# Performance work log

Hardware: AMD Instinct MI355X
Metric: run time of the kernel (lower is better)

The kernel has to match this reference:

```python
import jax, jax.numpy as jnp
import numpy as np


def _fir_kernel():
    # StyleGAN-2 low-pass FIR: outer([1,3,3,1]) normalized to sum 1
    k1 = jnp.array([1.0, 3.0, 3.0, 1.0], dtype=jnp.float32)
    k2 = jnp.outer(k1, k1)
    return k2 / k2.sum()


def setup_inputs() -> dict:
    key = jax.random.key(0)
    kx, kw = jax.random.split(key, 2)
    B, H, W, C, OC = 8, 128, 128, 128, 128
    x = jax.random.normal(kx, (B, H, W, C), dtype=jnp.float32)
    conv_w = jax.random.normal(kw, (3, 3, C, OC), dtype=jnp.float32) * 0.02  # HWIO
    conv_b = jnp.zeros((OC,), dtype=jnp.float32)
    return {"x": x, "conv_w": conv_w, "conv_b": conv_b}


def _upsample_fir(x):
    B, H, W, C = x.shape
    kernel = _fir_kernel()
    x_up = jnp.zeros((B, 2 * H, 2 * W, C), dtype=x.dtype)
    x_up = x_up.at[:, ::2, ::2, :].set(x)
    k = jnp.tile(kernel[None, None, :, :], (C, 1, 1, 1))  # OIHW, O=C, I=1
    y = jax.lax.conv_general_dilated(
        jnp.transpose(x_up, (0, 3, 1, 2)),  # NCHW
        k * 4.0,
        window_strides=(1, 1),
        padding="SAME",
        feature_group_count=C,
    )
    return jnp.transpose(y, (0, 2, 3, 1))  # back to NHWC


def reference(x, conv_w, conv_b):
    x_up = _upsample_fir(x)  # (B, 2H, 2W, C)
    out = jax.lax.conv_general_dilated(
        x_up,
        conv_w,
        window_strides=(1, 1),
        padding="SAME",
        dimension_numbers=("NHWC", "HWIO", "NHWC"),
    )
    return out + conv_b
```

## Files before the change

### kernel.cpp

```cpp
#include <hip/hip_runtime.h>

typedef __bf16 bf16x8 __attribute__((ext_vector_type(8)));
typedef float f32x4 __attribute__((ext_vector_type(4)));
typedef unsigned short ushort8 __attribute__((ext_vector_type(8)));

__device__ __forceinline__ unsigned short f2bf(float f) {
  unsigned int u = __builtin_bit_cast(unsigned int, f);
  u += 0x7FFFu + ((u >> 16) & 1u);
  return (unsigned short)(u >> 16);
}

__constant__ float COEF[2][3][3] = {
    {{0.25f, 0.00f, 0.00f},
     {0.75f, 0.75f, 0.25f},
     {0.00f, 0.25f, 0.75f}},
    {{0.75f, 0.25f, 0.00f},
     {0.25f, 0.75f, 0.75f},
     {0.00f, 0.00f, 0.25f}}
};

__global__ void pack_weights(const float* __restrict__ w, unsigned short* __restrict__ pw) {
  const int kt = blockIdx.x >> 3, nt = blockIdx.x & 7;
  const int l = threadIdx.x;
  const int tap = kt >> 2, cblk = kt & 3;
  const int du = tap / 3, dv = tap - du * 3;
  const int c0 = cblk * 32 + ((l >> 4) << 3);
  const int oc = nt * 16 + (l & 15);
  float accp[4][8];
#pragma unroll
  for (int ph = 0; ph < 4; ++ph)
#pragma unroll
    for (int j = 0; j < 8; ++j) accp[ph][j] = 0.0f;
#pragma unroll
  for (int u = 0; u < 3; ++u)
#pragma unroll
    for (int v = 0; v < 3; ++v) {
      const float ra0 = COEF[0][du][u], ra1 = COEF[1][du][u];
      const float cb0 = COEF[0][dv][v], cb1 = COEF[1][dv][v];
      const float c00 = ra0 * cb0, c01 = ra0 * cb1, c10 = ra1 * cb0, c11 = ra1 * cb1;
#pragma unroll
      for (int j = 0; j < 8; ++j) {
        const float wv = w[((u * 3 + v) * 128 + c0 + j) * 128 + oc];
        accp[0][j] += c00 * wv;
        accp[1][j] += c01 * wv;
        accp[2][j] += c10 * wv;
        accp[3][j] += c11 * wv;
      }
    }
  const int fi = ((cblk * 3 + dv) * 3 + du) * 8 + nt;
#pragma unroll
  for (int ph = 0; ph < 4; ++ph) {
    ushort8 o;
#pragma unroll
    for (int j = 0; j < 8; ++j) o[j] = f2bf(accp[ph][j]);
    *(ushort8*)(pw + (((ph * 288 + fi) * 64 + l) << 3)) = o;
  }
}

__global__ __launch_bounds__(512, 2) void fused_all(
    const float* __restrict__ x, const unsigned short* __restrict__ pw,
    const float* __restrict__ w, const float* __restrict__ bias,
    float* __restrict__ out) {
  __shared__ __align__(16) char smem[11 * 19 * 256];

  const int bid = blockIdx.x;
  const int tid = threadIdx.x;

  if (bid < 512) {
    const int chunk = bid & 31;
    const int type = (bid >> 5) & 1;
    const int bi = bid >> 6;
    const int base0 = chunk * 8;
    const float* xb = x + bi * (128 * 128 * 128);

    float* yw = (float*)smem;
    float* part = (float*)(smem + 16384);

    {
      const int c = tid & 127;
      const int sub = tid >> 7;
      for (int k = sub; k < 20; k += 4) {
        const int f = k / 10;
        const int ws = k - f * 10;
        const int t = base0 - 1 + ws;
        float val = 0.0f;
        if ((unsigned)t < 256u) {
          const int t0 = t >> 1;
          const float hA0 = (t & 1) ? 0.25f : 0.75f;
          const float hA1 = 1.0f - hA0;
          const float hF0 = f ? 0.25f : 0.75f;
          const float hF1 = 1.0f - hF0;
          const bool ok = (t0 + 1) < 128;
          if (type == 0) {
            const float v00 = xb[t0 * 128 + c];
            const float v01 = ok ? xb[(t0 + 1) * 128 + c] : 0.0f;
            const float v10 = xb[(128 + t0) * 128 + c];
            const float v11 = ok ? xb[(128 + t0 + 1) * 128 + c] : 0.0f;
            val = hF0 * (hA0 * v00 + hA1 * v01) + hF1 * (hA0 * v10 + hA1 * v11);
          } else {
            const float v00 = xb[(t0 * 128) * 128 + c];
            const float v01 = xb[(t0 * 128 + 1) * 128 + c];
            const float v10 = ok ? xb[((t0 + 1) * 128) * 128 + c] : 0.0f;
            const float v11 = ok ? xb[((t0 + 1) * 128 + 1) * 128 + c] : 0.0f;
            val = hA0 * (hF0 * v00 + hF1 * v01) + hA1 * (hF0 * v10 + hF1 * v11);
          }
        }
        yw[(f * 10 + ws) * 128 + c] = val;
      }
    }
    __syncthreads();

    const int wv = tid >> 6;
    const int oc0 = (tid & 63) * 2;
    const int cbase = wv * 16;

    float acc[8][2] = {};
#pragma unroll 1
    for (int cc = 0; cc < 16; ++cc) {
      float yr[2][10];
#pragma unroll
      for (int f = 0; f < 2; ++f)
#pragma unroll
        for (int ws = 0; ws < 10; ++ws)
          yr[f][ws] = yw[(f * 10 + ws) * 128 + cbase + cc];
#pragma unroll
      for (int tf = 0; tf < 2; ++tf) {
#pragma unroll
        for (int tb = 0; tb < 3; ++tb) {
          const int uu = (type == 0) ? (tf + 1) : tb;
          const int vv = (type == 0) ? tb : (tf + 1);
          const float2 w2 = *(const float2*)(
              w + ((uu * 3 + vv) * 128 + cbase + cc) * 128 + oc0);
#pragma unroll
          for (int pos = 0; pos < 8; ++pos) {
            const float yv = yr[tf][pos + tb];
            acc[pos][0] += yv * w2.x;
            acc[pos][1] += yv * w2.y;
          }
        }
      }
    }

#pragma unroll
    for (int pos = 0; pos < 8; ++pos)
      *(float2*)(part + (wv * 8 + pos) * 128 + oc0) = *(float2*)acc[pos];
    __syncthreads();

    const int pos = tid >> 6;
    const int ocp = (tid & 63) * 2;
    float s0 = 0.0f, s1 = 0.0f;
#pragma unroll
    for (int w8 = 0; w8 < 8; ++w8) {
      const float2 v = *(const float2*)(part + (w8 * 8 + pos) * 128 + ocp);
      s0 += v.x; s1 += v.y;
    }
    const int posg = base0 + pos;
    if (!(type == 1 && posg == 0)) {
      const int p = (type == 0) ? 0 : posg;
      const int q = (type == 0) ? posg : 0;
      const float2 b2 = *(const float2*)(bias + ocp);
      float2 r; r.x = s0 + b2.x; r.y = s1 + b2.y;
      *(float2*)(out + bi * (256 * 256 * 128) + (p * 256 + q) * 128 + ocp) = r;
    }
    return;
  }

  char* xlds = smem;
  const int o = bid - 512;
  const int blk = (o & 7) * 128 + (o >> 3);
  const int bimg = blk >> 7;
  const int it = (blk >> 3) & 15;
  const int jt = blk & 7;
  const int I0 = it * 8, J0 = jt * 16;
  const float* xb = x + bimg * (128 * 128 * 128);

  const int lane = tid & 63;
  const int l15 = lane & 15;
  const int lh = lane >> 4;
  const int wid = tid >> 6;
  const int a = (wid >> 2) & 1;
  const int b = (wid >> 1) & 1;
  const int nhalf = wid & 1;
  const int ph = a * 2 + b;

  const char* pwb = (const char*)pw + ph * 294912 + nhalf * 4096 + lane * 16;

#define LOADB(buf, g_, du_)                                           \
  do {                                                                \
    const char* bp_ = pwb + (((g_) * 3 + (du_)) << 13);               \
    _Pragma("unroll") for (int n = 0; n < 4; ++n)                     \
        buf[n] = *(const bf16x8*)(bp_ + n * 1024);                    \
  } while (0)

  bf16x8 b0[4], b1[4], b2[4];
  LOADB(b0, 0, 0);

  for (int idx = tid; idx < 11 * 19 * 16; idx += 512) {
    const int cp = idx & 15;
    const int pos = idx >> 4;
    const int xr = pos / 19;
    const int xc = pos - xr * 19;
    const int gi = I0 - 1 + xr;
    const int gj = J0 - 1 + xc;
    ushort8 u8 = {};
    if (((unsigned)gi < 128u) && ((unsigned)gj < 128u)) {
      const float* p = xb + ((gi << 7) + gj) * 128 + (cp << 3);
      const float4 A = *(const float4*)p;
      const float4 Bv = *(const float4*)(p + 4);
      u8[0] = f2bf(A.x); u8[1] = f2bf(A.y); u8[2] = f2bf(A.z); u8[3] = f2bf(A.w);
      u8[4] = f2bf(Bv.x); u8[5] = f2bf(Bv.y); u8[6] = f2bf(Bv.z); u8[7] = f2bf(Bv.w);
    }
    int byte = (pos << 8) + (cp << 4);
    byte ^= (pos & 7) << 4;
    *(ushort8*)(xlds + byte) = u8;
  }
  __syncthreads();

  f32x4 acc[8][4] = {};
  const int colpart = l15 + b;

#pragma unroll 1
  for (int g = 0; g < 12; ++g) {
    const int cblk = (g * 11) >> 5;
    const int dv = g - cblk * 3;
    const int kbyte = (cblk * 4 + lh) << 4;
    const int pbase = a * 19 + colpart + dv;

    bf16x8 af[10];
#define AREAD(rr)                                                     \
    do {                                                              \
      const int posa = pbase + (rr) * 19;                             \
      int byte_ = (posa << 8) + kbyte;                                \
      byte_ ^= (posa & 7) << 4;                \
      af[rr] = *(const bf16x8*)(xlds + byte_);                        \
    } while (0)

    AREAD(0); AREAD(1); AREAD(2); AREAD(3);
    AREAD(4); AREAD(5); AREAD(6); AREAD(7);
    LOADB(b1, g, 1);
    AREAD(8); AREAD(9);
    LOADB(b2, g, 2);

    __builtin_amdgcn_s_setprio(1);
#pragma unroll
    for (int m = 0; m < 8; ++m)
#pragma unroll
      for (int n = 0; n < 4; ++n)
        acc[m][n] = __builtin_amdgcn_mfma_f32_16x16x32_bf16(af[m], b0[n], acc[m][n], 0, 0, 0);
    __builtin_amdgcn_s_setprio(0);

    {
      const int gn = (g < 11) ? (g + 1) : 11;
      LOADB(b0, gn, 0);
    }

    __builtin_amdgcn_s_setprio(1);
#pragma unroll
    for (int m = 0; m < 8; ++m)
#pragma unroll
      for (int n = 0; n < 4; ++n)
        acc[m][n] = __builtin_amdgcn_mfma_f32_16x16x32_bf16(af[m + 1], b1[n], acc[m][n], 0, 0, 0);

#pragma unroll
    for (int m = 0; m < 8; ++m)
#pragma unroll
      for (int n = 0; n < 4; ++n)
        acc[m][n] = __builtin_amdgcn_mfma_f32_16x16x32_bf16(af[m + 2], b2[n], acc[m][n], 0, 0, 0);
    __builtin_amdgcn_s_setprio(0);
#undef AREAD
  }
#undef LOADB

  float bv[4];
#pragma unroll
  for (int n = 0; n < 4; ++n) bv[n] = bias[nhalf * 64 + n * 16 + l15];
  float* ob = out + bimg * (256 * 256 * 128) + nhalf * 64 + l15;
#pragma unroll
  for (int m = 0; m < 8; ++m) {
    const int p = it * 16 + 2 * m + a;
    if (p == 0) continue;
#pragma unroll
    for (int jr = 0; jr < 4; ++jr) {
      const int q = jt * 32 + 2 * (lh * 4 + jr) + b;
      if (q == 0) continue;
      float* orow = ob + (p * 256 + q) * 128;
#pragma unroll
      for (int n = 0; n < 4; ++n) orow[n * 16] = acc[m][n][jr] + bv[n];
    }
  }
}

extern "C" void kernel_launch(void* const* d_in, const int* in_sizes, int n_in,
                              void* d_out, int out_size, void* d_ws, size_t ws_size,
                              hipStream_t stream) {
  const float* x = (const float*)d_in[0];
  const float* w = (const float*)d_in[1];
  const float* bias = (const float*)d_in[2];
  float* out = (float*)d_out;
  unsigned short* pw = (unsigned short*)d_ws;

  pack_weights<<<dim3(288), dim3(64), 0, stream>>>(w, pw);
  fused_all<<<dim3(1536), dim3(512), 0, stream>>>(x, pw, w, bias, out);
}
```

Before: 172.1 us.

## Halve row tile to 256-thread blocks, each wave covering all 128 output channels

Shrinks the main conv tile from 8 to 4 input rows with 256-thread blocks (4 waves) instead of 512. Each wave now computes all 128 output channels (8 N-fragments) over 4 M-rows rather than splitting channels across wave pairs. The weight prefetch becomes a two-buffer ping-pong across an unrolled pair of groups. The aim is less LDS per block, more blocks for load balance, and more B reuse per A read. In exchange, each wave holds more accumulator and weight registers, and each block carries a larger relative halo in the x tile.

```diff
diff --git a/kernel.cpp b/kernel.cpp
--- a/kernel.cpp
+++ b/kernel.cpp
@@ -57,11 +57,11 @@
   }
 }
 
-__global__ __launch_bounds__(512, 2) void fused_all(
+__global__ __launch_bounds__(256, 2) void fused_all(
     const float* __restrict__ x, const unsigned short* __restrict__ pw,
     const float* __restrict__ w, const float* __restrict__ bias,
     float* __restrict__ out) {
-  __shared__ __align__(16) char smem[11 * 19 * 256];
+  __shared__ __align__(16) char smem[7 * 19 * 256];
 
   const int bid = blockIdx.x;
   const int tid = threadIdx.x;
@@ -74,12 +74,12 @@
     const float* xb = x + bi * (128 * 128 * 128);
 
     float* yw = (float*)smem;
-    float* part = (float*)(smem + 16384);
+    float* part = (float*)(smem + 10240);
 
     {
       const int c = tid & 127;
       const int sub = tid >> 7;
-      for (int k = sub; k < 20; k += 4) {
+      for (int k = sub; k < 20; k += 2) {
         const int f = k / 10;
         const int ws = k - f * 10;
         const int t = base0 - 1 + ws;
@@ -112,11 +112,11 @@
 
     const int wv = tid >> 6;
     const int oc0 = (tid & 63) * 2;
-    const int cbase = wv * 16;
+    const int cbase = wv * 32;
 
     float acc[8][2] = {};
 #pragma unroll 1
-    for (int cc = 0; cc < 16; ++cc) {
+    for (int cc = 0; cc < 32; ++cc) {
       float yr[2][10];
 #pragma unroll
       for (int f = 0; f < 2; ++f)
@@ -146,56 +146,56 @@
       *(float2*)(part + (wv * 8 + pos) * 128 + oc0) = *(float2*)acc[pos];
     __syncthreads();
 
-    const int pos = tid >> 6;
-    const int ocp = (tid & 63) * 2;
-    float s0 = 0.0f, s1 = 0.0f;
-#pragma unroll
-    for (int w8 = 0; w8 < 8; ++w8) {
-      const float2 v = *(const float2*)(part + (w8 * 8 + pos) * 128 + ocp);
-      s0 += v.x; s1 += v.y;
+    const int pos = tid >> 5;
+    const int ocp = (tid & 31) * 4;
+    float4 s = {0.f, 0.f, 0.f, 0.f};
+#pragma unroll
+    for (int w4i = 0; w4i < 4; ++w4i) {
+      const float4 v = *(const float4*)(part + (w4i * 8 + pos) * 128 + ocp);
+      s.x += v.x; s.y += v.y; s.z += v.z; s.w += v.w;
     }
     const int posg = base0 + pos;
     if (!(type == 1 && posg == 0)) {
       const int p = (type == 0) ? 0 : posg;
       const int q = (type == 0) ? posg : 0;
-      const float2 b2 = *(const float2*)(bias + ocp);
-      float2 r; r.x = s0 + b2.x; r.y = s1 + b2.y;
-      *(float2*)(out + bi * (256 * 256 * 128) + (p * 256 + q) * 128 + ocp) = r;
+      const float4 b4 = *(const float4*)(bias + ocp);
+      float4 r;
+      r.x = s.x + b4.x; r.y = s.y + b4.y; r.z = s.z + b4.z; r.w = s.w + b4.w;
+      *(float4*)(out + bi * (256 * 256 * 128) + (p * 256 + q) * 128 + ocp) = r;
     }
     return;
   }
 
   char* xlds = smem;
   const int o = bid - 512;
-  const int blk = (o & 7) * 128 + (o >> 3);
-  const int bimg = blk >> 7;
-  const int it = (blk >> 3) & 15;
+  const int blk = (o & 7) * 256 + (o >> 3);
+  const int bimg = blk >> 8;
+  const int it = (blk >> 3) & 31;
   const int jt = blk & 7;
-  const int I0 = it * 8, J0 = jt * 16;
+  const int I0 = it * 4, J0 = jt * 16;
   const float* xb = x + bimg * (128 * 128 * 128);
 
   const int lane = tid & 63;
   const int l15 = lane & 15;
   const int lh = lane >> 4;
   const int wid = tid >> 6;
-  const int a = (wid >> 2) & 1;
-  const int b = (wid >> 1) & 1;
-  const int nhalf = wid & 1;
+  const int a = wid >> 1;
+  const int b = wid & 1;
   const int ph = a * 2 + b;
 
-  const char* pwb = (const char*)pw + ph * 294912 + nhalf * 4096 + lane * 16;
+  const char* pwb = (const char*)pw + ph * 294912 + lane * 16;
 
 #define LOADB(buf, g_, du_)                                           \
   do {                                                                \
     const char* bp_ = pwb + (((g_) * 3 + (du_)) << 13);               \
-    _Pragma("unroll") for (int n = 0; n < 4; ++n)                     \
+    _Pragma("unroll") for (int n = 0; n < 8; ++n)                     \
         buf[n] = *(const bf16x8*)(bp_ + n * 1024);                    \
   } while (0)
 
-  bf16x8 b0[4], b1[4], b2[4];
-  LOADB(b0, 0, 0);
-
-  for (int idx = tid; idx < 11 * 19 * 16; idx += 512) {
+  bf16x8 bX[8], bY[8];
+  LOADB(bX, 0, 0);
+
+  for (int idx = tid; idx < 7 * 19 * 16; idx += 256) {
     const int cp = idx & 15;
     const int pos = idx >> 4;
     const int xr = pos / 19;
@@ -216,68 +216,73 @@
   }
   __syncthreads();
 
-  f32x4 acc[8][4] = {};
+  f32x4 acc[4][8] = {};
   const int colpart = l15 + b;
 
+#define AREAD(rr, dv_)                                                \
+  do {                                                                \
+    const int posa = (a + (rr)) * 19 + colpart + (dv_);               \
+    int byte_ = (posa << 8) + kbyte;                                  \
+    byte_ ^= (posa & 7) << 4;                  \
+    af[rr] = *(const bf16x8*)(xlds + byte_);                          \
+  } while (0)
+
+#define MFMAS(du_, buf)                                               \
+  do {                                                                \
+    __builtin_amdgcn_s_setprio(1);                                    \
+    _Pragma("unroll") for (int m = 0; m < 4; ++m)                     \
+        _Pragma("unroll") for (int n = 0; n < 8; ++n)                 \
+            acc[m][n] = __builtin_amdgcn_mfma_f32_16x16x32_bf16(      \
+                af[(du_) + m], buf[n], acc[m][n], 0, 0, 0);           \
+    __builtin_amdgcn_s_setprio(0);                                    \
+  } while (0)
+
 #pragma unroll 1
-  for (int g = 0; g < 12; ++g) {
-    const int cblk = (g * 11) >> 5;
-    const int dv = g - cblk * 3;
-    const int kbyte = (cblk * 4 + lh) << 4;
-    const int pbase = a * 19 + colpart + dv;
-
-    bf16x8 af[10];
-#define AREAD(rr)                                                     \
-    do {                                                              \
-      const int posa = pbase + (rr) * 19;                             \
-      int byte_ = (posa << 8) + kbyte;                                \
-      byte_ ^= (posa & 7) << 4;                \
-      af[rr] = *(const bf16x8*)(xlds + byte_);                        \
-    } while (0)
-
-    AREAD(0); AREAD(1); AREAD(2); AREAD(3);
-    AREAD(4); AREAD(5); AREAD(6); AREAD(7);
-    LOADB(b1, g, 1);
-    AREAD(8); AREAD(9);
-    LOADB(b2, g, 2);
-
-    __builtin_amdgcn_s_setprio(1);
-#pragma unroll
-    for (int m = 0; m < 8; ++m)
-#pragma unroll
-      for (int n = 0; n < 4; ++n)
-        acc[m][n] = __builtin_amdgcn_mfma_f32_16x16x32_bf16(af[m], b0[n], acc[m][n], 0, 0, 0);
-    __builtin_amdgcn_s_setprio(0);
-
+  for (int g = 0; g < 12; g += 2) {
     {
-      const int gn = (g < 11) ? (g + 1) : 11;
-      LOADB(b0, gn, 0);
-    }
-
-    __builtin_amdgcn_s_setprio(1);
-#pragma unroll
-    for (int m = 0; m < 8; ++m)
-#pragma unroll
-      for (int n = 0; n < 4; ++n)
-        acc[m][n] = __builtin_amdgcn_mfma_f32_16x16x32_bf16(af[m + 1], b1[n], acc[m][n], 0, 0, 0);
-
-#pragma unroll
-    for (int m = 0; m < 8; ++m)
-#pragma unroll
-      for (int n = 0; n < 4; ++n)
-        acc[m][n] = __builtin_amdgcn_mfma_f32_16x16x32_bf16(af[m + 2], b2[n], acc[m][n], 0, 0, 0);
-    __builtin_amdgcn_s_setprio(0);
+      const int cblk = (g * 11) >> 5;
+      const int dv = g - cblk * 3;
+      const int kbyte = (cblk * 4 + lh) << 4;
+      bf16x8 af[6];
+      AREAD(0, dv); AREAD(1, dv); AREAD(2, dv);
+      AREAD(3, dv); AREAD(4, dv); AREAD(5, dv);
+      LOADB(bY, g, 1);
+      MFMAS(0, bX);
+      LOADB(bX, g, 2);
+      MFMAS(1, bY);
+      LOADB(bY, g + 1, 0);
+      MFMAS(2, bX);
+    }
+    {
+      const int g1 = g + 1;
+      const int cblk = (g1 * 11) >> 5;
+      const int dv = g1 - cblk * 3;
+      const int kbyte = (cblk * 4 + lh) << 4;
+      bf16x8 af[6];
+      AREAD(0, dv); AREAD(1, dv); AREAD(2, dv);
+      AREAD(3, dv); AREAD(4, dv); AREAD(5, dv);
+      LOADB(bX, g1, 1);
+      MFMAS(0, bY);
+      LOADB(bY, g1, 2);
+      MFMAS(1, bX);
+      {
+        const int gn = (g + 2 < 12) ? (g + 2) : 11;
+        LOADB(bX, gn, 0);
+      }
+      MFMAS(2, bY);
+    }
+  }
 #undef AREAD
-  }
+#undef MFMAS
 #undef LOADB
 
-  float bv[4];
-#pragma unroll
-  for (int n = 0; n < 4; ++n) bv[n] = bias[nhalf * 64 + n * 16 + l15];
-  float* ob = out + bimg * (256 * 256 * 128) + nhalf * 64 + l15;
-#pragma unroll
-  for (int m = 0; m < 8; ++m) {
-    const int p = it * 16 + 2 * m + a;
+  float bv[8];
+#pragma unroll
+  for (int n = 0; n < 8; ++n) bv[n] = bias[n * 16 + l15];
+  float* ob = out + bimg * (256 * 256 * 128) + l15;
+#pragma unroll
+  for (int m = 0; m < 4; ++m) {
+    const int p = it * 8 + 2 * m + a;
     if (p == 0) continue;
 #pragma unroll
     for (int jr = 0; jr < 4; ++jr) {
@@ -285,7 +290,7 @@
       if (q == 0) continue;
       float* orow = ob + (p * 256 + q) * 128;
 #pragma unroll
-      for (int n = 0; n < 4; ++n) orow[n * 16] = acc[m][n][jr] + bv[n];
+      for (int n = 0; n < 8; ++n) orow[n * 16] = acc[m][n][jr] + bv[n];
     }
   }
 }
@@ -300,5 +305,5 @@
   unsigned short* pw = (unsigned short*)d_ws;
 
   pack_weights<<<dim3(288), dim3(64), 0, stream>>>(w, pw);
-  fused_all<<<dim3(1536), dim3(512), 0, stream>>>(x, pw, w, bias, out);
+  fused_all<<<dim3(2560), dim3(256), 0, stream>>>(x, pw, w, bias, out);
 }
```

New measurement: 178.1 us. 3.5% more time.

## Switch main conv to 32x32x16 MFMA with 4x32 spatial tiles

Applied to the files above, without the earlier changes.

The main conv path moves from 16x16x32 bf16 MFMA to 32x32x16 MFMA. Each block now covers a 4x32 input tile (a 7x35 halo in LDS) instead of 8x16, and the K loop is split into 24 half-steps. The pre-packed weight layout is reorganised to match the new B-fragment shape. The goal is fewer LDS A-fragment reads per FLOP and higher MFMA efficiency, at the cost of a wider halo, a slightly larger LDS footprint, and changed output store patterns.

```diff
diff --git a/kernel.cpp b/kernel.cpp
--- a/kernel.cpp
+++ b/kernel.cpp
@@ -1,7 +1,7 @@
 #include <hip/hip_runtime.h>
 
 typedef __bf16 bf16x8 __attribute__((ext_vector_type(8)));
-typedef float f32x4 __attribute__((ext_vector_type(4)));
+typedef float f32x16 __attribute__((ext_vector_type(16)));
 typedef unsigned short ushort8 __attribute__((ext_vector_type(8)));
 
 __device__ __forceinline__ unsigned short f2bf(float f) {
@@ -20,12 +20,16 @@
 };
 
 __global__ void pack_weights(const float* __restrict__ w, unsigned short* __restrict__ pw) {
-  const int kt = blockIdx.x >> 3, nt = blockIdx.x & 7;
+  const int fi = blockIdx.x;
   const int l = threadIdx.x;
-  const int tap = kt >> 2, cblk = kt & 3;
-  const int du = tap / 3, dv = tap - du * 3;
-  const int c0 = cblk * 32 + ((l >> 4) << 3);
-  const int oc = nt * 16 + (l & 15);
+  const int nt32 = fi & 3;
+  int t = fi >> 2;
+  const int du = t % 3; t /= 3;
+  const int ksub = t & 1; t >>= 1;
+  const int dv = t % 3;
+  const int cblk = t / 3;
+  const int c0 = cblk * 32 + ksub * 16 + ((l >> 5) << 3);
+  const int oc = nt32 * 32 + (l & 31);
   float accp[4][8];
 #pragma unroll
   for (int ph = 0; ph < 4; ++ph)
@@ -47,7 +51,6 @@
         accp[3][j] += c11 * wv;
       }
     }
-  const int fi = ((cblk * 3 + dv) * 3 + du) * 8 + nt;
 #pragma unroll
   for (int ph = 0; ph < 4; ++ph) {
     ushort8 o;
@@ -61,7 +64,7 @@
     const float* __restrict__ x, const unsigned short* __restrict__ pw,
     const float* __restrict__ w, const float* __restrict__ bias,
     float* __restrict__ out) {
-  __shared__ __align__(16) char smem[11 * 19 * 256];
+  __shared__ __align__(16) char smem[7 * 35 * 256];
 
   const int bid = blockIdx.x;
   const int tid = threadIdx.x;
@@ -169,37 +172,37 @@
   const int o = bid - 512;
   const int blk = (o & 7) * 128 + (o >> 3);
   const int bimg = blk >> 7;
-  const int it = (blk >> 3) & 15;
-  const int jt = blk & 7;
-  const int I0 = it * 8, J0 = jt * 16;
+  const int it = (blk >> 2) & 31;
+  const int jt = blk & 3;
+  const int I0 = it * 4, J0 = jt * 32;
   const float* xb = x + bimg * (128 * 128 * 128);
 
   const int lane = tid & 63;
-  const int l15 = lane & 15;
-  const int lh = lane >> 4;
+  const int l31 = lane & 31;
+  const int khalf = lane >> 5;
   const int wid = tid >> 6;
   const int a = (wid >> 2) & 1;
   const int b = (wid >> 1) & 1;
-  const int nhalf = wid & 1;
+  const int nh = wid & 1;
   const int ph = a * 2 + b;
 
-  const char* pwb = (const char*)pw + ph * 294912 + nhalf * 4096 + lane * 16;
-
-#define LOADB(buf, g_, du_)                                           \
+  const char* pwb = (const char*)pw + ph * 294912 + (nh * 2) * 1024 + lane * 16;
+
+#define LOADB(buf, gg_, du_)                                          \
   do {                                                                \
-    const char* bp_ = pwb + (((g_) * 3 + (du_)) << 13);               \
-    _Pragma("unroll") for (int n = 0; n < 4; ++n)                     \
-        buf[n] = *(const bf16x8*)(bp_ + n * 1024);                    \
+    const char* bp_ = pwb + (((gg_) * 3 + (du_)) << 12);              \
+    buf[0] = *(const bf16x8*)(bp_);                                   \
+    buf[1] = *(const bf16x8*)(bp_ + 1024);                            \
   } while (0)
 
-  bf16x8 b0[4], b1[4], b2[4];
+  bf16x8 b0[2], b1[2], b2[2];
   LOADB(b0, 0, 0);
 
-  for (int idx = tid; idx < 11 * 19 * 16; idx += 512) {
+  for (int idx = tid; idx < 7 * 35 * 16; idx += 512) {
     const int cp = idx & 15;
     const int pos = idx >> 4;
-    const int xr = pos / 19;
-    const int xc = pos - xr * 19;
+    const int xr = pos / 35;
+    const int xc = pos - xr * 35;
     const int gi = I0 - 1 + xr;
     const int gj = J0 - 1 + xc;
     ushort8 u8 = {};
@@ -216,76 +219,69 @@
   }
   __syncthreads();
 
-  f32x4 acc[8][4] = {};
-  const int colpart = l15 + b;
+  f32x16 acc[4][2] = {};
+  const int colpart = l31 + b;
+
+#define AREAD(rr, dv_, kbyte_)                                        \
+  do {                                                                \
+    const int posa = (a + (rr)) * 35 + colpart + (dv_);               \
+    int byte_ = (posa << 8) + (kbyte_);                               \
+    byte_ ^= (posa & 7) << 4;                  \
+    af[rr] = *(const bf16x8*)(xlds + byte_);                          \
+  } while (0)
+
+#define MFMAS(du_, buf)                                               \
+  do {                                                                \
+    __builtin_amdgcn_s_setprio(1);                                    \
+    _Pragma("unroll") for (int mt = 0; mt < 4; ++mt)                  \
+        _Pragma("unroll") for (int n = 0; n < 2; ++n)                 \
+            acc[mt][n] = __builtin_amdgcn_mfma_f32_32x32x16_bf16(     \
+                af[(du_) + mt], buf[n], acc[mt][n], 0, 0, 0);         \
+    __builtin_amdgcn_s_setprio(0);                                    \
+  } while (0)
 
 #pragma unroll 1
-  for (int g = 0; g < 12; ++g) {
-    const int cblk = (g * 11) >> 5;
-    const int dv = g - cblk * 3;
-    const int kbyte = (cblk * 4 + lh) << 4;
-    const int pbase = a * 19 + colpart + dv;
-
-    bf16x8 af[10];
-#define AREAD(rr)                                                     \
-    do {                                                              \
-      const int posa = pbase + (rr) * 19;                             \
-      int byte_ = (posa << 8) + kbyte;                                \
-      byte_ ^= (posa & 7) << 4;                \
-      af[rr] = *(const bf16x8*)(xlds + byte_);                        \
-    } while (0)
-
-    AREAD(0); AREAD(1); AREAD(2); AREAD(3);
-    AREAD(4); AREAD(5); AREAD(6); AREAD(7);
-    LOADB(b1, g, 1);
-    AREAD(8); AREAD(9);
-    LOADB(b2, g, 2);
-
-    __builtin_amdgcn_s_setprio(1);
-#pragma unroll
-    for (int m = 0; m < 8; ++m)
-#pragma unroll
-      for (int n = 0; n < 4; ++n)
-        acc[m][n] = __builtin_amdgcn_mfma_f32_16x16x32_bf16(af[m], b0[n], acc[m][n], 0, 0, 0);
-    __builtin_amdgcn_s_setprio(0);
-
+  for (int gg = 0; gg < 24; ++gg) {
+    const int gd = gg >> 1;
+    const int ksub = gg & 1;
+    const int cblk = gd / 3;
+    const int dv = gd - cblk * 3;
+    const int kbyte = cblk * 64 + ksub * 32 + (khalf << 4);
+
+    bf16x8 af[6];
+    AREAD(0, dv, kbyte); AREAD(1, dv, kbyte); AREAD(2, dv, kbyte);
+    AREAD(3, dv, kbyte); AREAD(4, dv, kbyte); AREAD(5, dv, kbyte);
+
+    LOADB(b1, gg, 1);
+    MFMAS(0, b0);
+    LOADB(b2, gg, 2);
+    MFMAS(1, b1);
     {
-      const int gn = (g < 11) ? (g + 1) : 11;
+      const int gn = (gg < 23) ? (gg + 1) : 23;
       LOADB(b0, gn, 0);
     }
-
-    __builtin_amdgcn_s_setprio(1);
-#pragma unroll
-    for (int m = 0; m < 8; ++m)
-#pragma unroll
-      for (int n = 0; n < 4; ++n)
-        acc[m][n] = __builtin_amdgcn_mfma_f32_16x16x32_bf16(af[m + 1], b1[n], acc[m][n], 0, 0, 0);
-
-#pragma unroll
-    for (int m = 0; m < 8; ++m)
-#pragma unroll
-      for (int n = 0; n < 4; ++n)
-        acc[m][n] = __builtin_amdgcn_mfma_f32_16x16x32_bf16(af[m + 2], b2[n], acc[m][n], 0, 0, 0);
-    __builtin_amdgcn_s_setprio(0);
+    MFMAS(2, b2);
+  }
 #undef AREAD
-  }
+#undef MFMAS
 #undef LOADB
 
-  float bv[4];
-#pragma unroll
-  for (int n = 0; n < 4; ++n) bv[n] = bias[nhalf * 64 + n * 16 + l15];
-  float* ob = out + bimg * (256 * 256 * 128) + nhalf * 64 + l15;
-#pragma unroll
-  for (int m = 0; m < 8; ++m) {
-    const int p = it * 16 + 2 * m + a;
+  float bv[2];
+  bv[0] = bias[nh * 64 + l31];
+  bv[1] = bias[nh * 64 + 32 + l31];
+  float* ob = out + bimg * (256 * 256 * 128) + nh * 64 + l31;
+#pragma unroll
+  for (int mt = 0; mt < 4; ++mt) {
+    const int p = it * 8 + 2 * mt + a;
     if (p == 0) continue;
 #pragma unroll
-    for (int jr = 0; jr < 4; ++jr) {
-      const int q = jt * 32 + 2 * (lh * 4 + jr) + b;
+    for (int reg = 0; reg < 16; ++reg) {
+      const int row = (reg & 3) + 8 * (reg >> 2) + 4 * khalf;
+      const int q = jt * 64 + 2 * row + b;
       if (q == 0) continue;
       float* orow = ob + (p * 256 + q) * 128;
-#pragma unroll
-      for (int n = 0; n < 4; ++n) orow[n * 16] = acc[m][n][jr] + bv[n];
+      orow[0]  = acc[mt][0][reg] + bv[0];
+      orow[32] = acc[mt][1][reg] + bv[1];
     }
   }
 }
```

Measured after the change: 197.6 us. +14.8%, slower.

## Stage input tile via direct global-to-LDS loads in fp32, convert on read

Applied to the files above, without the earlier changes.

Replaces the register-staged fp32-to-bf16 conversion of the input halo tile with asynchronous global_load_lds transfers that write raw fp32 into LDS. Out-of-bounds positions are served from a zeroed scratch buffer written by pack_weights. Conversion to bf16 moves into the A-fragment reads inside the MFMA loop. LDS usage roughly doubles (about 105 KB), which may cut occupancy below the two-blocks-per-CU launch bound, and the inner loop now does two LDS reads plus a conversion per fragment.

```diff
diff --git a/kernel.cpp b/kernel.cpp
--- a/kernel.cpp
+++ b/kernel.cpp
@@ -22,6 +22,7 @@
 __global__ void pack_weights(const float* __restrict__ w, unsigned short* __restrict__ pw) {
   const int kt = blockIdx.x >> 3, nt = blockIdx.x & 7;
   const int l = threadIdx.x;
+  if (blockIdx.x == 0 && l < 16) ((float*)(pw + 589824))[l] = 0.0f;
   const int tap = kt >> 2, cblk = kt & 3;
   const int du = tap / 3, dv = tap - du * 3;
   const int c0 = cblk * 32 + ((l >> 4) << 3);
@@ -60,8 +61,8 @@
 __global__ __launch_bounds__(512, 2) void fused_all(
     const float* __restrict__ x, const unsigned short* __restrict__ pw,
     const float* __restrict__ w, const float* __restrict__ bias,
-    float* __restrict__ out) {
-  __shared__ __align__(16) char smem[11 * 19 * 256];
+    float* __restrict__ out, const float* __restrict__ zp) {
+  __shared__ __align__(16) char smem[210 * 512];
 
   const int bid = blockIdx.x;
   const int tid = threadIdx.x;
@@ -195,80 +196,79 @@
   bf16x8 b0[4], b1[4], b2[4];
   LOADB(b0, 0, 0);
 
-  for (int idx = tid; idx < 11 * 19 * 16; idx += 512) {
-    const int cp = idx & 15;
-    const int pos = idx >> 4;
-    const int xr = pos / 19;
-    const int xc = pos - xr * 19;
-    const int gi = I0 - 1 + xr;
-    const int gj = J0 - 1 + xc;
-    ushort8 u8 = {};
-    if (((unsigned)gi < 128u) && ((unsigned)gj < 128u)) {
-      const float* p = xb + ((gi << 7) + gj) * 128 + (cp << 3);
-      const float4 A = *(const float4*)p;
-      const float4 Bv = *(const float4*)(p + 4);
-      u8[0] = f2bf(A.x); u8[1] = f2bf(A.y); u8[2] = f2bf(A.z); u8[3] = f2bf(A.w);
-      u8[4] = f2bf(Bv.x); u8[5] = f2bf(Bv.y); u8[6] = f2bf(Bv.z); u8[7] = f2bf(Bv.w);
-    }
-    int byte = (pos << 8) + (cp << 4);
-    byte ^= (pos & 7) << 4;
-    *(ushort8*)(xlds + byte) = u8;
+  {
+    const int k = lane & 31;
+    const int ph2 = lane >> 5;
+    for (int item = wid; item < 105; item += 8) {
+      const int p = item * 2 + ph2;
+      const int xr = p / 19, xc = p - xr * 19;
+      const int gi = I0 - 1 + xr, gj = J0 - 1 + xc;
+      const int kk = k ^ (p & 15);
+      const float* src;
+      if (((unsigned)gi < 128u) && ((unsigned)gj < 128u) && (xr < 11))
+        src = xb + ((gi << 7) + gj) * 128 + (kk << 2);
+      else
+        src = zp;
+      __builtin_amdgcn_global_load_lds(
+          (const __attribute__((address_space(1))) unsigned int*)src,
+          (__attribute__((address_space(3))) unsigned int*)(xlds + item * 1024),
+          16, 0, 0);
+    }
   }
   __syncthreads();
 
   f32x4 acc[8][4] = {};
   const int colpart = l15 + b;
+
+#define AREAD(rr, dv_, tq_)                                                     \
+  do {                                                                          \
+    const int posa = (a + (rr)) * 19 + colpart + (dv_);                         \
+    const int sw = posa & 15;                                                   \
+    const char* pbase = xlds + (posa << 9);                                     \
+    const int co = (((tq_) << 1) ^ sw) << 4;                                    \
+    const f32x4 lo = *(const f32x4*)(pbase + co);                               \
+    const f32x4 hi = *(const f32x4*)(pbase + (co ^ 16));                        \
+    bf16x8 t_;                                                                  \
+    t_[0] = (__bf16)lo[0]; t_[1] = (__bf16)lo[1];                               \
+    t_[2] = (__bf16)lo[2]; t_[3] = (__bf16)lo[3];                               \
+    t_[4] = (__bf16)hi[0]; t_[5] = (__bf16)hi[1];                               \
+    t_[6] = (__bf16)hi[2]; t_[7] = (__bf16)hi[3];                               \
+    af[rr] = t_;                                                                \
+  } while (0)
+
+#define MFMAS(du_, buf)                                               \
+  do {                                                                \
+    __builtin_amdgcn_s_setprio(1);                                    \
+    _Pragma("unroll") for (int m = 0; m < 8; ++m)                     \
+        _Pragma("unroll") for (int n = 0; n < 4; ++n)                 \
+            acc[m][n] = __builtin_amdgcn_mfma_f32_16x16x32_bf16(      \
+                af[(du_) + m], buf[n], acc[m][n], 0, 0, 0);           \
+    __builtin_amdgcn_s_setprio(0);                                    \
+  } while (0)
 
 #pragma unroll 1
   for (int g = 0; g < 12; ++g) {
     const int cblk = (g * 11) >> 5;
     const int dv = g - cblk * 3;
-    const int kbyte = (cblk * 4 + lh) << 4;
-    const int pbase = a * 19 + colpart + dv;
+    const int tq = cblk * 4 + lh;
 
     bf16x8 af[10];
-#define AREAD(rr)                                                     \
-    do {                                                              \
-      const int posa = pbase + (rr) * 19;                             \
-      int byte_ = (posa << 8) + kbyte;                                \
-      byte_ ^= (posa & 7) << 4;                \
-      af[rr] = *(const bf16x8*)(xlds + byte_);                        \
-    } while (0)
-
-    AREAD(0); AREAD(1); AREAD(2); AREAD(3);
-    AREAD(4); AREAD(5); AREAD(6); AREAD(7);
+    AREAD(0, dv, tq); AREAD(1, dv, tq); AREAD(2, dv, tq); AREAD(3, dv, tq);
+    AREAD(4, dv, tq); AREAD(5, dv, tq); AREAD(6, dv, tq); AREAD(7, dv, tq);
     LOADB(b1, g, 1);
-    AREAD(8); AREAD(9);
+    AREAD(8, dv, tq); AREAD(9, dv, tq);
     LOADB(b2, g, 2);
 
-    __builtin_amdgcn_s_setprio(1);
-#pragma unroll
-    for (int m = 0; m < 8; ++m)
-#pragma unroll
-      for (int n = 0; n < 4; ++n)
-        acc[m][n] = __builtin_amdgcn_mfma_f32_16x16x32_bf16(af[m], b0[n], acc[m][n], 0, 0, 0);
-    __builtin_amdgcn_s_setprio(0);
-
+    MFMAS(0, b0);
     {
       const int gn = (g < 11) ? (g + 1) : 11;
       LOADB(b0, gn, 0);
     }
-
-    __builtin_amdgcn_s_setprio(1);
-#pragma unroll
-    for (int m = 0; m < 8; ++m)
-#pragma unroll
-      for (int n = 0; n < 4; ++n)
-        acc[m][n] = __builtin_amdgcn_mfma_f32_16x16x32_bf16(af[m + 1], b1[n], acc[m][n], 0, 0, 0);
-
-#pragma unroll
-    for (int m = 0; m < 8; ++m)
-#pragma unroll
-      for (int n = 0; n < 4; ++n)
-        acc[m][n] = __builtin_amdgcn_mfma_f32_16x16x32_bf16(af[m + 2], b2[n], acc[m][n], 0, 0, 0);
-    __builtin_amdgcn_s_setprio(0);
+    MFMAS(1, b1);
+    MFMAS(2, b2);
+  }
 #undef AREAD
-  }
+#undef MFMAS
 #undef LOADB
 
   float bv[4];
@@ -298,7 +298,8 @@
   const float* bias = (const float*)d_in[2];
   float* out = (float*)d_out;
   unsigned short* pw = (unsigned short*)d_ws;
+  const float* zp = (const float*)((char*)d_ws + 1179648);
 
   pack_weights<<<dim3(288), dim3(64), 0, stream>>>(w, pw);
-  fused_all<<<dim3(1536), dim3(512), 0, stream>>>(x, pw, w, bias, out);
+  fused_all<<<dim3(1536), dim3(512), 0, stream>>>(x, pw, w, bias, out, zp);
 }
```

Result: slower. 184.8 us (+7.4%).
